# Kernel optimization log

Measured on AMD Instinct MI355X. Metric: run time of the kernel, lower is better.

The kernel has to match this reference:

```python
import jax, jax.numpy as jnp
import numpy as np

B = 16384      # batch of states
N = 64         # neighbors per state -> x width = 5 + 2*N = 133
H = 128        # embed / hidden feature dim (num_inputs)
HID = 256      # actor/critic hidden size
OUT = 2        # action dim


def setup_inputs() -> dict:
    key = jax.random.key(0)
    ks = jax.random.split(key, 12)
    w = lambda k, shp: (jax.random.normal(k, shp, jnp.float32) * 0.1)
    b = lambda n: jnp.full((n,), 0.1, jnp.float32)
    return {
        "x": jax.random.normal(ks[0], (B, 5 + 2 * N), jnp.float32),
        # embbedLayer: Linear(2,128)
        "We": w(ks[1], (H, 2)), "be": b(H),
        # hlayer: Linear(128,128)
        "Wh": w(ks[2], (H, H)), "bh": b(H),
        # attentionLayer: Linear(256,1)
        "Wa": w(ks[3], (1, 2 * H)), "ba": b(1),
        # layer2: Linear(133,128)
        "W2": w(ks[4], (H, H + 5)), "b2": b(H),
        # critic: Linear(128,256) -> Linear(256,1)
        "Wc1": w(ks[5], (HID, H)), "bc1": b(HID),
        "Wc2": w(ks[6], (1, HID)), "bc2": b(1),
        # actor: Linear(128,256) -> Linear(256,2)
        "Wp1": w(ks[7], (HID, H)), "bp1": b(HID),
        "Wp2": w(ks[8], (OUT, HID)), "bp2": b(OUT),
        # log_std parameter (std=0.0 -> ones*0.0)
        "log_std": jnp.zeros((1, OUT), jnp.float32),
    }


def reference(x, We, be, Wh, bh, Wa, ba, W2, b2,
              Wc1, bc1, Wc2, bc2, Wp1, bp1, Wp2, bp2, log_std):
    Bn = x.shape[0]
    state_loc = x[:, :5]                       # [B,5]
    nb = x[:, 5:].reshape(Bn, -1, 2)           # [B,N,2] ragged loop flattened

    e = jax.nn.relu(jnp.einsum('bnd,hd->bnh', nb, We) + be)   # [B,N,H]
    em = jnp.mean(e, axis=1, keepdims=True)                    # [B,1,H]
    h = jax.nn.relu(jnp.einsum('bnh,oh->bno', e, Wh) + bh)     # [B,N,H]

    # attentionLayer(hstack(e, em)): split Wa into e-part and mean-part
    Wa_e, Wa_m = Wa[:, :H], Wa[:, H:]
    score = jax.nn.relu(
        jnp.einsum('bnh,oh->bno', e, Wa_e)
        + jnp.einsum('bkh,oh->bko', em, Wa_m)   # [B,1,1] broadcasts over N
        + ba
    )                                            # [B,N,1]
    attn = jax.nn.softmax(score, axis=1)         # softmax over neighbors
    mean_feature = jnp.mean(attn * h, axis=1)    # [B,H]

    t = jax.nn.relu(
        jnp.concatenate([state_loc, mean_feature], axis=1) @ W2.T + b2
    )                                            # [B,H]

    value = jax.nn.relu(t @ Wc1.T + bc1) @ Wc2.T + bc2   # [B,1]
    mu = jax.nn.relu(t @ Wp1.T + bp1) @ Wp2.T + bp2       # [B,2]
    std = jnp.broadcast_to(jnp.exp(log_std), mu.shape)    # [B,2]
    return mu, std, value
```

## Files before the change

### kernel.cpp

```cpp
#include <hip/hip_runtime.h>

#define BATCH 16384
#define XDIM  133
#define RPB   2
#define EROW  272
#define MB    64
#define CROW  336
#define TROW  272

#define WH_OFF   0
#define W2_OFF   16384
#define WC1_OFF  36864
#define WP1_OFF  69632
#define WA_OFF   102400
#define WE2_OFF  102528
#define MFG_OFF  208896

typedef __attribute__((ext_vector_type(8))) _Float16 half8;
typedef __attribute__((ext_vector_type(4))) _Float16 half4v;
typedef __attribute__((ext_vector_type(2))) _Float16 half2v;
typedef __attribute__((ext_vector_type(4))) float    f32x4;
typedef __attribute__((ext_vector_type(4))) unsigned int uint4v;

__device__ __forceinline__ float relu(float v) { return fmaxf(v, 0.f); }
__device__ __forceinline__ unsigned short f2h(float f) {
    _Float16 h = (_Float16)f;
    return __builtin_bit_cast(unsigned short, h);
}
__device__ __forceinline__ half2v pk2h(float a, float b) {
    return __builtin_bit_cast(half2v, __builtin_amdgcn_cvt_pkrtz(a, b));
}

__global__ __launch_bounds__(256)
void ac_prep(const float* __restrict__ Wh, const float* __restrict__ W2,
             const float* __restrict__ Wc1, const float* __restrict__ Wp1,
             const float* __restrict__ Wa, const float* __restrict__ We,
             const float* __restrict__ be, unsigned short* __restrict__ wsH)
{
    const int idx = blockIdx.x * 256 + threadIdx.x;
    const int stride = gridDim.x * 256;
    for (int i = idx; i < 128*128; i += stride) wsH[WH_OFF + i] = f2h(Wh[i]);
    for (int i = idx; i < 128*160; i += stride) {
        int o = i / 160, ck = i - o*160;
        float w = (ck < 128) ? W2[o*XDIM + 5 + ck]
                             : ((ck < 133) ? W2[o*XDIM + (ck - 128)] : 0.f);
        wsH[W2_OFF + i] = f2h(w);
    }
    for (int i = idx; i < 256*128; i += stride) wsH[WC1_OFF + i] = f2h(Wc1[i]);
    for (int i = idx; i < 256*128; i += stride) wsH[WP1_OFF + i] = f2h(Wp1[i]);
    for (int i = idx; i < 128;     i += stride) wsH[WA_OFF  + i] = f2h(Wa[i]);
    for (int hp = idx; hp < 128;   hp += stride) {
        wsH[WE2_OFF + hp*8 + 0] = f2h(We[4*hp+0]);
        wsH[WE2_OFF + hp*8 + 1] = f2h(We[4*hp+2]);
        wsH[WE2_OFF + hp*8 + 2] = f2h(We[4*hp+1]);
        wsH[WE2_OFF + hp*8 + 3] = f2h(We[4*hp+3]);
        wsH[WE2_OFF + hp*8 + 4] = f2h(be[2*hp+0]);
        wsH[WE2_OFF + hp*8 + 5] = f2h(be[2*hp+1]);
        wsH[WE2_OFF + hp*8 + 6] = f2h(Wa[128+2*hp+0]);
        wsH[WE2_OFF + hp*8 + 7] = f2h(Wa[128+2*hp+1]);
    }
}

__global__ __launch_bounds__(256, 4)
void ac_attn(const float* __restrict__ x,
             const float* __restrict__ bh,  const float* __restrict__ ba,
             const unsigned short* __restrict__ wsH,
             char* __restrict__ mfG)
{
    __shared__ __align__(16) char  eH[RPB * 64 * EROW];
    __shared__ __align__(16) char  xsH[RPB * 64 * 8];
    __shared__            float cpart[4][RPB];

    const int tid  = threadIdx.x;
    const int lane = tid & 63;
    const int wave = tid >> 6;
    const int b0   = blockIdx.x * RPB;

    if (tid < 128) {
        int r = tid >> 6, n = tid & 63;
        float2 nb = *(const float2*)(x + (size_t)(b0 + r) * XDIM + 5 + 2*n);
        half2v s0 = pk2h(nb.x, nb.x);
        half2v s1 = pk2h(nb.y, nb.y);
        half4v s; s[0] = s0[0]; s[1] = s0[1]; s[2] = s1[0]; s[3] = s1[1];
        *(half4v*)(xsH + (r*64 + n)*8) = s;
    }
    __syncthreads();

    {
        const int hp = lane;
        const int q  = wave;
        half8 wp = *(const half8*)(wsH + WE2_OFF + hp*8);
        half2v W0 = {wp[0], wp[1]};
        half2v W1 = {wp[2], wp[3]};
        half2v BE = {wp[4], wp[5]};
        half2v WAM = {wp[6], wp[7]};
        const half2v Z = {(_Float16)0.0f, (_Float16)0.0f};
        #pragma unroll
        for (int r = 0; r < RPB; ++r) {
            float ca = 0.f;
            #pragma unroll
            for (int i = 0; i < 16; ++i) {
                int n = q*16 + i;
                half4v s = *(const half4v*)(xsH + (r*64 + n)*8);
                half2v s0 = {s[0], s[1]};
                half2v s1 = {s[2], s[3]};
                half2v X = s0*W0 + BE;
                X = s1*W1 + X;
                X = __builtin_elementwise_max(X, Z);
                ca = __builtin_amdgcn_fdot2(X, WAM, ca, false);
                *(half2v*)(eH + (r*64 + n)*EROW + (hp << 2)) = X;
            }
            #pragma unroll
            for (int off = 1; off < 64; off <<= 1) ca += __shfl_xor(ca, off);
            if (lane == 0) cpart[wave][r] = ca;
        }
    }
    __syncthreads();

    {
        const int lo = lane & 15;
        const int g  = lane >> 4;
        const int r  = wave >> 1;
        const int ch = wave & 1;

        float s = 0.f;
        {
            const int row = r*64 + lane;
            const half2v* wa = (const half2v*)(wsH + WA_OFF);
            #pragma unroll
            for (int k16 = 0; k16 < 16; ++k16) {
                half8 v = *(const half8*)(eH + row*EROW + k16*16);
                const half2v* v2 = (const half2v*)&v;
                #pragma unroll
                for (int j = 0; j < 4; ++j)
                    s = __builtin_amdgcn_fdot2(v2[j], wa[k16*4 + j], s, false);
            }
        }
        const float cterm = (cpart[0][r] + cpart[1][r] + cpart[2][r] + cpart[3][r])
                            * (1.f/64.f) + ba[0];
        float sc = relu(s + cterm);
        float m = sc;
        #pragma unroll
        for (int off = 1; off < 64; off <<= 1) m = fmaxf(m, __shfl_xor(m, off));
        float p = __expf(sc - m);
        float sum = p;
        #pragma unroll
        for (int off = 1; off < 64; off <<= 1) sum += __shfl_xor(sum, off);
        const float attn = p / (sum * 64.f);

        const unsigned short* WhH = wsH + WH_OFF;
        #pragma unroll
        for (int cp = 0; cp < 2; ++cp) {
            const int c0 = ch*64 + cp*32 + lo;
            const int c1 = c0 + 16;
            half8 bfr[2][4];
            #pragma unroll
            for (int kk = 0; kk < 4; ++kk) {
                bfr[0][kk] = *(const half8*)(WhH + (size_t)c0*128 + kk*32 + g*8);
                bfr[1][kk] = *(const half8*)(WhH + (size_t)c1*128 + kk*32 + g*8);
            }
            const float bh0 = bh[c0], bh1 = bh[c1];
            float mf0 = 0.f, mf1 = 0.f;
            #pragma unroll
            for (int nt = 0; nt < 4; ++nt) {
                const int arow = r*64 + nt*16 + lo;
                half8 af[4];
                #pragma unroll
                for (int kk = 0; kk < 4; ++kk)
                    af[kk] = *(const half8*)(eH + arow*EROW + kk*64 + g*16);
                f32x4 acc0 = {0.f,0.f,0.f,0.f};
                f32x4 acc1 = {0.f,0.f,0.f,0.f};
                #pragma unroll
                for (int kk = 0; kk < 4; ++kk) {
                    acc0 = __builtin_amdgcn_mfma_f32_16x16x32_f16(af[kk], bfr[0][kk], acc0, 0, 0, 0);
                    acc1 = __builtin_amdgcn_mfma_f32_16x16x32_f16(af[kk], bfr[1][kk], acc1, 0, 0, 0);
                }
                float at[4];
                #pragma unroll
                for (int j = 0; j < 4; ++j)
                    at[j] = __shfl(attn, nt*16 + g*4 + j);
                #pragma unroll
                for (int j = 0; j < 4; ++j) {
                    mf0 = fmaf(at[j], relu(acc0[j] + bh0), mf0);
                    mf1 = fmaf(at[j], relu(acc1[j] + bh1), mf1);
                }
            }
            mf0 += __shfl_xor(mf0, 16);  mf0 += __shfl_xor(mf0, 32);
            mf1 += __shfl_xor(mf1, 16);  mf1 += __shfl_xor(mf1, 32);
            if (lane < 16) {
                size_t base = (size_t)(b0 + r)*128 + ch*64 + cp*32 + lane;
                *(unsigned short*)(mfG + base*2)        = f2h(mf0);
                *(unsigned short*)(mfG + (base + 16)*2) = f2h(mf1);
            }
        }
    }
}

__global__ __launch_bounds__(256, 1)
void ac_heads(const float* __restrict__ x, const char* __restrict__ mfG,
              const unsigned short* __restrict__ wsH,
              const float* __restrict__ b2,
              const float* __restrict__ bc1, const float* __restrict__ Wc2,
              const float* __restrict__ bc2,
              const float* __restrict__ bp1, const float* __restrict__ Wp2,
              const float* __restrict__ bp2,
              const float* __restrict__ log_std,
              float* __restrict__ out)
{
    __shared__ __align__(16) char catS[MB * CROW];
    __shared__ __align__(16) char tS[MB * TROW];
    __shared__ float redV [2][MB];
    __shared__ float redM0[2][MB];
    __shared__ float redM1[2][MB];

    const int tid  = threadIdx.x;
    const int lane = tid & 63;
    const int wave = tid >> 6;
    const int lo   = lane & 15;
    const int g    = lane >> 4;
    const int b0   = blockIdx.x * MB;

    for (int i = tid * 16; i < MB * CROW; i += 256 * 16)
        *(uint4v*)(catS + i) = (uint4v){0, 0, 0, 0};
    __syncthreads();
    for (int c = tid; c < MB * 16; c += 256) {
        int row = c >> 4, sl = c & 15;
        uint4v v = *(const uint4v*)(mfG + (size_t)(b0 + row) * 256 + sl * 16);
        *(uint4v*)(catS + row * CROW + sl * 16) = v;
    }
    for (int m = tid; m < MB; m += 256) {
        const float* xr = x + (size_t)(b0 + m) * XDIM;
        #pragma unroll
        for (int k = 0; k < 5; ++k)
            *(unsigned short*)(catS + m * CROW + 256 + 2*k) = f2h(xr[k]);
    }
    __syncthreads();

    {
        const int o = wave * 32 + lo;
        const unsigned short* W2H = wsH + W2_OFF;
        half8 bw[2][5];
        #pragma unroll
        for (int nt2 = 0; nt2 < 2; ++nt2)
            #pragma unroll
            for (int kk = 0; kk < 5; ++kk)
                bw[nt2][kk] = *(const half8*)(W2H + (size_t)(o + nt2*16)*160 + kk*32 + g*8);
        const float bb0 = b2[o], bb1 = b2[o + 16];
        #pragma unroll
        for (int mt = 0; mt < 4; ++mt) {
            const int arow = mt*16 + lo;
            half8 af[5];
            #pragma unroll
            for (int kk = 0; kk < 5; ++kk)
                af[kk] = *(const half8*)(catS + arow*CROW + kk*64 + g*16);
            f32x4 a0 = {0.f,0.f,0.f,0.f}, a1 = {0.f,0.f,0.f,0.f};
            #pragma unroll
            for (int kk = 0; kk < 5; ++kk) {
                a0 = __builtin_amdgcn_mfma_f32_16x16x32_f16(af[kk], bw[0][kk], a0, 0, 0, 0);
                a1 = __builtin_amdgcn_mfma_f32_16x16x32_f16(af[kk], bw[1][kk], a1, 0, 0, 0);
            }
            #pragma unroll
            for (int j = 0; j < 4; ++j) {
                int m = mt*16 + g*4 + j;
                *(unsigned short*)(tS + m*TROW + o*2)      = f2h(relu(a0[j] + bb0));
                *(unsigned short*)(tS + m*TROW + (o+16)*2) = f2h(relu(a1[j] + bb1));
            }
        }
    }
    __syncthreads();

    {
        const bool isval = (wave < 2);
        const unsigned short* W1H = wsH + (isval ? WC1_OFF : WP1_OFF);
        const float* bb = isval ? bc1 : bp1;
        const int obase = (wave & 1) * 128;
        float sA[4][4], sB[4][4];
        #pragma unroll
        for (int mt = 0; mt < 4; ++mt)
            #pragma unroll
            for (int j = 0; j < 4; ++j) { sA[mt][j] = 0.f; sB[mt][j] = 0.f; }

        #pragma unroll
        for (int np = 0; np < 4; ++np) {
            const int oA = obase + np*32 + lo;
            const int oB = oA + 16;
            half8 bf0[4], bf1[4];
            #pragma unroll
            for (int kk = 0; kk < 4; ++kk) {
                bf0[kk] = *(const half8*)(W1H + (size_t)oA*128 + kk*32 + g*8);
                bf1[kk] = *(const half8*)(W1H + (size_t)oB*128 + kk*32 + g*8);
            }
            const float biasA = bb[oA], biasB = bb[oB];
            float wA0, wB0, wA1 = 0.f, wB1 = 0.f;
            if (isval) { wA0 = Wc2[oA]; wB0 = Wc2[oB]; }
            else       { wA0 = Wp2[oA]; wB0 = Wp2[oB]; wA1 = Wp2[256+oA]; wB1 = Wp2[256+oB]; }

            #pragma unroll
            for (int mt = 0; mt < 4; ++mt) {
                const int arow = mt*16 + lo;
                half8 af[4];
                #pragma unroll
                for (int kk = 0; kk < 4; ++kk)
                    af[kk] = *(const half8*)(tS + arow*TROW + kk*64 + g*16);
                f32x4 a0 = {0.f,0.f,0.f,0.f}, a1 = {0.f,0.f,0.f,0.f};
                #pragma unroll
                for (int kk = 0; kk < 4; ++kk) {
                    a0 = __builtin_amdgcn_mfma_f32_16x16x32_f16(af[kk], bf0[kk], a0, 0, 0, 0);
                    a1 = __builtin_amdgcn_mfma_f32_16x16x32_f16(af[kk], bf1[kk], a1, 0, 0, 0);
                }
                #pragma unroll
                for (int j = 0; j < 4; ++j) {
                    float uA = relu(a0[j] + biasA);
                    float uB = relu(a1[j] + biasB);
                    sA[mt][j] += wA0*uA + wB0*uB;
                    sB[mt][j] += wA1*uA + wB1*uB;
                }
            }
        }
        #pragma unroll
        for (int mt = 0; mt < 4; ++mt)
            #pragma unroll
            for (int j = 0; j < 4; ++j) {
                #pragma unroll
                for (int off = 1; off < 16; off <<= 1) {
                    sA[mt][j] += __shfl_xor(sA[mt][j], off);
                    sB[mt][j] += __shfl_xor(sB[mt][j], off);
                }
            }
        if (lo == 0) {
            #pragma unroll
            for (int mt = 0; mt < 4; ++mt)
                #pragma unroll
                for (int j = 0; j < 4; ++j) {
                    int m = mt*16 + g*4 + j;
                    if (isval) redV[wave][m] = sA[mt][j];
                    else { redM0[wave-2][m] = sA[mt][j]; redM1[wave-2][m] = sB[mt][j]; }
                }
        }
    }
    __syncthreads();

    if (tid < MB) {
        const int m = tid;
        const int b = b0 + m;
        out[b*2 + 0]           = redM0[0][m] + redM0[1][m] + bp2[0];
        out[b*2 + 1]           = redM1[0][m] + redM1[1][m] + bp2[1];
        out[2*BATCH + b*2 + 0] = expf(log_std[0]);
        out[2*BATCH + b*2 + 1] = expf(log_std[1]);
        out[4*BATCH + b]       = redV[0][m] + redV[1][m] + bc2[0];
    }
}

extern "C" void kernel_launch(void* const* d_in, const int* in_sizes, int n_in,
                              void* d_out, int out_size, void* d_ws, size_t ws_size,
                              hipStream_t stream) {
    (void)in_sizes; (void)n_in; (void)ws_size; (void)out_size;
    const float* x       = (const float*)d_in[0];
    const float* We      = (const float*)d_in[1];
    const float* be      = (const float*)d_in[2];
    const float* Wh      = (const float*)d_in[3];
    const float* bh      = (const float*)d_in[4];
    const float* Wa      = (const float*)d_in[5];
    const float* ba      = (const float*)d_in[6];
    const float* W2      = (const float*)d_in[7];
    const float* b2      = (const float*)d_in[8];
    const float* Wc1     = (const float*)d_in[9];
    const float* bc1     = (const float*)d_in[10];
    const float* Wc2     = (const float*)d_in[11];
    const float* bc2     = (const float*)d_in[12];
    const float* Wp1     = (const float*)d_in[13];
    const float* bp1     = (const float*)d_in[14];
    const float* Wp2     = (const float*)d_in[15];
    const float* bp2     = (const float*)d_in[16];
    const float* log_std = (const float*)d_in[17];

    unsigned short* wsH = (unsigned short*)d_ws;
    char* mfG = (char*)d_ws + MFG_OFF;

    hipLaunchKernelGGL(ac_prep, dim3(64), dim3(256), 0, stream,
                       Wh, W2, Wc1, Wp1, Wa, We, be, wsH);
    hipLaunchKernelGGL(ac_attn, dim3(BATCH / RPB), dim3(256), 0, stream,
                       x, bh, ba, wsH, mfG);
    hipLaunchKernelGGL(ac_heads, dim3(BATCH / MB), dim3(256), 0, stream,
                       x, mfG, wsH, b2, bc1, Wc2, bc2, bp1, Wp2, bp2,
                       log_std, (float*)d_out);
}
```

Measured before the change: 95.68 us.

## Fuse attention score into MFMA loop with online softmax per wave

Computes the attention scores with an MFMA against a zero-padded Wa column (only lane lo==0 holds real weights) instead of a separate fdot2 pass, and switches to an online softmax with running max and rescaling that is merged across lane groups at the end. Work is repartitioned so each wave owns 32 output channels across both rows, which keeps the Wh fragments resident and loads them once. This removes the separate score pass and its full-wave max/sum reductions, but adds extra exps for rescaling and redundant score MFMAs in every wave.

```diff
diff --git a/kernel.cpp b/kernel.cpp
--- a/kernel.cpp
+++ b/kernel.cpp
@@ -120,47 +120,31 @@
     {
         const int lo = lane & 15;
         const int g  = lane >> 4;
-        const int r  = wave >> 1;
-        const int ch = wave & 1;
-
-        float s = 0.f;
-        {
-            const int row = r*64 + lane;
-            const half2v* wa = (const half2v*)(wsH + WA_OFF);
-            #pragma unroll
-            for (int k16 = 0; k16 < 16; ++k16) {
-                half8 v = *(const half8*)(eH + row*EROW + k16*16);
-                const half2v* v2 = (const half2v*)&v;
-                #pragma unroll
-                for (int j = 0; j < 4; ++j)
-                    s = __builtin_amdgcn_fdot2(v2[j], wa[k16*4 + j], s, false);
-            }
-        }
-        const float cterm = (cpart[0][r] + cpart[1][r] + cpart[2][r] + cpart[3][r])
-                            * (1.f/64.f) + ba[0];
-        float sc = relu(s + cterm);
-        float m = sc;
-        #pragma unroll
-        for (int off = 1; off < 64; off <<= 1) m = fmaxf(m, __shfl_xor(m, off));
-        float p = __expf(sc - m);
-        float sum = p;
-        #pragma unroll
-        for (int off = 1; off < 64; off <<= 1) sum += __shfl_xor(sum, off);
-        const float attn = p / (sum * 64.f);
-
+        const int c0 = wave*32 + lo;
+        const int c1 = c0 + 16;
         const unsigned short* WhH = wsH + WH_OFF;
-        #pragma unroll
-        for (int cp = 0; cp < 2; ++cp) {
-            const int c0 = ch*64 + cp*32 + lo;
-            const int c1 = c0 + 16;
-            half8 bfr[2][4];
-            #pragma unroll
-            for (int kk = 0; kk < 4; ++kk) {
-                bfr[0][kk] = *(const half8*)(WhH + (size_t)c0*128 + kk*32 + g*8);
-                bfr[1][kk] = *(const half8*)(WhH + (size_t)c1*128 + kk*32 + g*8);
-            }
-            const float bh0 = bh[c0], bh1 = bh[c1];
+        half8 bfr[2][4];
+        #pragma unroll
+        for (int kk = 0; kk < 4; ++kk) {
+            int kb = kk*32 + g*8;
+            bfr[0][kk] = *(const half8*)(WhH + c0*128 + kb);
+            bfr[1][kk] = *(const half8*)(WhH + c1*128 + kb);
+        }
+        const half8 hz = {(_Float16)0.f,(_Float16)0.f,(_Float16)0.f,(_Float16)0.f,
+                          (_Float16)0.f,(_Float16)0.f,(_Float16)0.f,(_Float16)0.f};
+        half8 bsc[4];
+        #pragma unroll
+        for (int kk = 0; kk < 4; ++kk)
+            bsc[kk] = (lo == 0) ? *(const half8*)(wsH + WA_OFF + kk*32 + g*8) : hz;
+        const float bh0 = bh[c0], bh1 = bh[c1];
+
+        #pragma unroll
+        for (int r = 0; r < RPB; ++r) {
+            const float cterm = (cpart[0][r] + cpart[1][r] + cpart[2][r] + cpart[3][r])
+                                * (1.f/64.f) + ba[0];
+            float m = 0.f, lsum = 0.f;
             float mf0 = 0.f, mf1 = 0.f;
+
             #pragma unroll
             for (int nt = 0; nt < 4; ++nt) {
                 const int arow = r*64 + nt*16 + lo;
@@ -168,6 +152,17 @@
                 #pragma unroll
                 for (int kk = 0; kk < 4; ++kk)
                     af[kk] = *(const half8*)(eH + arow*EROW + kk*64 + g*16);
+
+                f32x4 sac = {0.f,0.f,0.f,0.f};
+                #pragma unroll
+                for (int kk = 0; kk < 4; ++kk)
+                    sac = __builtin_amdgcn_mfma_f32_16x16x32_f16(af[kk], bsc[kk], sac, 0, 0, 0);
+                float s_[4];
+                #pragma unroll
+                for (int j = 0; j < 4; ++j) s_[j] = relu(sac[j] + cterm);
+                #pragma unroll
+                for (int j = 0; j < 4; ++j) s_[j] = __shfl(s_[j], lane & 48);
+
                 f32x4 acc0 = {0.f,0.f,0.f,0.f};
                 f32x4 acc1 = {0.f,0.f,0.f,0.f};
                 #pragma unroll
@@ -175,22 +170,41 @@
                     acc0 = __builtin_amdgcn_mfma_f32_16x16x32_f16(af[kk], bfr[0][kk], acc0, 0, 0, 0);
                     acc1 = __builtin_amdgcn_mfma_f32_16x16x32_f16(af[kk], bfr[1][kk], acc1, 0, 0, 0);
                 }
-                float at[4];
-                #pragma unroll
-                for (int j = 0; j < 4; ++j)
-                    at[j] = __shfl(attn, nt*16 + g*4 + j);
+
+                float pm = fmaxf(fmaxf(s_[0], s_[1]), fmaxf(s_[2], s_[3]));
+                float mn = fmaxf(m, pm);
+                float resc = __expf(m - mn);
+                lsum *= resc;  mf0 *= resc;  mf1 *= resc;
+                float p_[4];
+                #pragma unroll
+                for (int j = 0; j < 4; ++j) p_[j] = __expf(s_[j] - mn);
+                lsum += p_[0] + p_[1] + p_[2] + p_[3];
                 #pragma unroll
                 for (int j = 0; j < 4; ++j) {
-                    mf0 = fmaf(at[j], relu(acc0[j] + bh0), mf0);
-                    mf1 = fmaf(at[j], relu(acc1[j] + bh1), mf1);
-                }
-            }
-            mf0 += __shfl_xor(mf0, 16);  mf0 += __shfl_xor(mf0, 32);
-            mf1 += __shfl_xor(mf1, 16);  mf1 += __shfl_xor(mf1, 32);
+                    mf0 = fmaf(p_[j], relu(acc0[j] + bh0), mf0);
+                    mf1 = fmaf(p_[j], relu(acc1[j] + bh1), mf1);
+                }
+                m = mn;
+            }
+
+            #pragma unroll
+            for (int off = 16; off <= 32; off <<= 1) {
+                float mo  = __shfl_xor(m, off);
+                float lo_ = __shfl_xor(lsum, off);
+                float f0  = __shfl_xor(mf0, off);
+                float f1  = __shfl_xor(mf1, off);
+                float mn = fmaxf(m, mo);
+                float a = __expf(m - mn), b = __expf(mo - mn);
+                lsum = lsum*a + lo_*b;
+                mf0  = mf0*a  + f0*b;
+                mf1  = mf1*a  + f1*b;
+                m = mn;
+            }
+            const float inv = 1.0f / (lsum * 64.f);
             if (lane < 16) {
-                size_t base = (size_t)(b0 + r)*128 + ch*64 + cp*32 + lane;
-                *(unsigned short*)(mfG + base*2)        = f2h(mf0);
-                *(unsigned short*)(mfG + (base + 16)*2) = f2h(mf1);
+                size_t base = (size_t)(b0 + r)*128 + wave*32 + lane;
+                *(unsigned short*)(mfG + base*2)        = f2h(mf0 * inv);
+                *(unsigned short*)(mfG + (base + 16)*2) = f2h(mf1 * inv);
             }
         }
     }
```

After: 92.21 us. 3.6% less time.
